# Performance work log

Hardware: AMD Instinct MI355X
Metric: run time of the kernel (lower is better)

Reference implementation:

```python
import jax, jax.numpy as jnp
import numpy as np

N_HEADS = 16
D_MODEL = 1024


def setup_inputs() -> dict:
    key = jax.random.key(0)
    ks = jax.random.split(key, 9)
    B, S, D = 2, 2048, D_MODEL
    scale = 1.0 / np.sqrt(D)
    inp = {
        "x": jax.random.normal(ks[0], (B, S, D), dtype=jnp.float32),
        "wq": jax.random.normal(ks[1], (D, D), dtype=jnp.float32) * scale,
        "bq": jax.random.normal(ks[2], (D,), dtype=jnp.float32) * 0.01,
        "wk": jax.random.normal(ks[3], (D, D), dtype=jnp.float32) * scale,
        "bk": jax.random.normal(ks[4], (D,), dtype=jnp.float32) * 0.01,
        "wv": jax.random.normal(ks[5], (D, D), dtype=jnp.float32) * scale,
        "bv": jax.random.normal(ks[6], (D,), dtype=jnp.float32) * 0.01,
        "wo": jax.random.normal(ks[7], (D, D), dtype=jnp.float32) * scale,
        "bo": jax.random.normal(ks[8], (D,), dtype=jnp.float32) * 0.01,
    }
    return inp


def reference(x, wq, bq, wk, bk, wv, bv, wo, bo):
    B, S, D = x.shape
    H = N_HEADS
    hd = D // H
    # projections -> [B, H, S, hd]
    def proj(w, b):
        return (x @ w + b).reshape(B, S, H, hd).transpose(0, 2, 1, 3)
    q = proj(wq, bq)
    k = proj(wk, bk)
    v = proj(wv, bv)
    scores = jnp.einsum("bhqd,bhkd->bhqk", q, k) * (1.0 / np.sqrt(hd))
    # causal mask: future tokens (col > row) -> -inf
    causal = jnp.tril(jnp.ones((S, S), dtype=bool))  # True = allowed
    scores = jnp.where(causal[None, None, :, :], scores, -jnp.inf)
    att = jax.nn.softmax(scores, axis=-1)
    y = jnp.einsum("bhqk,bhkd->bhqd", att, v)  # [B,H,S,hd]
    y = y.transpose(0, 2, 1, 3).reshape(B, S, D)
    return y @ wo + bo
```

## Files before the change

kernel.cpp:

```cpp
#include <hip/hip_runtime.h>
#include <hip/hip_bf16.h>
#include <math.h>

typedef unsigned short u16;
typedef __bf16 bf16x8 __attribute__((ext_vector_type(8)));
typedef short s16x4 __attribute__((ext_vector_type(4)));
typedef float f32x4 __attribute__((ext_vector_type(4)));
typedef u16 u16x8 __attribute__((ext_vector_type(8)));
typedef u16 u16x4 __attribute__((ext_vector_type(4)));

#define DM 1024
#define NH 16
#define SL 2048
#define BB 2
#define TOK (BB * SL)

__device__ __forceinline__ u16 f2bf(float f) {
  union { float f; unsigned u; } v; v.f = f;
  unsigned r = v.u + 0x7FFFu + ((v.u >> 16) & 1u);
  return (u16)(r >> 16);
}

__device__ __forceinline__ float fexp2(float x) {
  float r; asm("v_exp_f32 %0, %1" : "=v"(r) : "v"(x)); return r;
}

__device__ __forceinline__ unsigned cvtpk(float lo, float hi) {
  unsigned r;
  asm("v_cvt_pk_bf16_f32 %0, %1, %2" : "=v"(r) : "v"(lo), "v"(hi));
  return r;
}

__device__ __forceinline__ float max3f(float a, float b, float c) {
  return fmaxf(fmaxf(a, b), c);
}

__device__ __forceinline__ f32x4 pv_mfma(s16x4 a, s16x4 b, f32x4 c) {
#if __has_builtin(__builtin_amdgcn_mfma_f32_16x16x16bf16_1k)
  return __builtin_amdgcn_mfma_f32_16x16x16bf16_1k(a, b, c, 0, 0, 0);
#else
  asm("v_mfma_f32_16x16x16_bf16 %0, %1, %2, %0" : "+v"(c) : "v"(a), "v"(b));
  return c;
#endif
}

typedef __attribute__((address_space(1))) const unsigned GU;
typedef __attribute__((address_space(3))) unsigned LU;
#define GLOAD16(g, l) __builtin_amdgcn_global_load_lds((GU*)(g), (LU*)(l), 16, 0, 0)

__global__ __launch_bounds__(256) void prep(
    const float* __restrict__ x,
    const float* __restrict__ w0, const float* __restrict__ w1,
    const float* __restrict__ w2, const float* __restrict__ w3,
    u16* __restrict__ Xb, u16* __restrict__ Wall) {
  __shared__ u16 T[64][72];
  int bid = blockIdx.x;
  int tid = threadIdx.x;
  if (bid < 1024) {
    int mat = bid >> 8;
    const float* in = (mat == 0) ? w0 : (mat == 1) ? w1 : (mat == 2) ? w2 : w3;
    u16* o = Wall + ((size_t)mat << 20);
    int t2 = bid & 255;
    int k0 = (t2 & 15) * 64, n0 = (t2 >> 4) * 64;
    int r = tid >> 2;
    int c0 = (tid & 3) * 16;
#pragma unroll
    for (int j = 0; j < 16; j += 4) {
      float4 f = *(const float4*)(in + (size_t)(k0 + r) * 1024 + n0 + c0 + j);
      T[c0 + j + 0][r] = f2bf(f.x);
      T[c0 + j + 1][r] = f2bf(f.y);
      T[c0 + j + 2][r] = f2bf(f.z);
      T[c0 + j + 3][r] = f2bf(f.w);
    }
    __syncthreads();
    int n = tid >> 2, k1 = (tid & 3) * 16;
#pragma unroll
    for (int j = 0; j < 16; j += 8)
      *(u16x8*)(o + (size_t)(n0 + n) * 1024 + k0 + k1 + j) = *(const u16x8*)&T[n][k1 + j];
  } else {
    int i = ((bid - 1024) * 256 + tid) * 8;
    float4 a = *(const float4*)(x + i);
    float4 b = *(const float4*)(x + i + 4);
    u16x8 o;
    o[0]=f2bf(a.x); o[1]=f2bf(a.y); o[2]=f2bf(a.z); o[3]=f2bf(a.w);
    o[4]=f2bf(b.x); o[5]=f2bf(b.y); o[6]=f2bf(b.z); o[7]=f2bf(b.w);
    *(u16x8*)(Xb + i) = o;
  }
}

template<int MODE, int BM>
__global__ __launch_bounds__(256) void gemm_qkv(
    const u16* __restrict__ A, const u16* __restrict__ Bt,
    const float* __restrict__ b0, const float* __restrict__ b1,
    const float* __restrict__ b2,
    u16* __restrict__ Qo, u16* __restrict__ Ko, u16* __restrict__ Vto,
    float* __restrict__ Fo)
{
  constexpr int MREP = BM / 32;
  __shared__ u16 As[3][BM * 32];
  __shared__ u16 Bs[3][128 * 32];
  const int tid = threadIdx.x, lane = tid & 63, w = tid >> 6;
  const int fr = lane & 15, fq = lane >> 4;
  const int wr = w >> 1, wc = w & 1;
  const int m0 = blockIdx.x * BM;
  const int n0 = blockIdx.y * 128;
  f32x4 acc[MREP][4] = {};

  auto stage = [&](int buf, int k0) {
#pragma unroll
    for (int i = 0; i < BM / 64; ++i) {
      int b16 = i * 256 + tid;
      int row = b16 >> 2, ch = b16 & 3;
      GLOAD16(A + (size_t)(m0 + row) * DM + k0 + ((ch ^ (row & 3)) * 8), &As[buf][b16 * 8]);
    }
#pragma unroll
    for (int i = 0; i < 2; ++i) {
      int b16 = i * 256 + tid;
      int row = b16 >> 2, ch = b16 & 3;
      GLOAD16(Bt + (size_t)(n0 + row) * DM + k0 + ((ch ^ (row & 3)) * 8), &Bs[buf][b16 * 8]);
    }
  };

  const int NK = DM / 32;
  stage(0, 0);
  stage(1, 32);
  for (int j = 0; j < NK; ++j) {
    if (j + 1 < NK) {
      if constexpr (BM == 128) asm volatile("s_waitcnt vmcnt(4)" ::: "memory");
      else                     asm volatile("s_waitcnt vmcnt(3)" ::: "memory");
    } else {
      asm volatile("s_waitcnt vmcnt(0)" ::: "memory");
    }
    __builtin_amdgcn_s_barrier();
    __builtin_amdgcn_sched_barrier(0);

    const u16* Al = As[j % 3];
    const u16* Bl = Bs[j % 3];
    bf16x8 av[MREP], bv[4];
#pragma unroll
    for (int m = 0; m < MREP; ++m) {
      int row = wr * (BM / 2) + m * 16 + fr;
      av[m] = *(const bf16x8*)&Al[row * 32 + ((fq ^ (row & 3)) * 8)];
    }
#pragma unroll
    for (int n = 0; n < 4; ++n) {
      int row = wc * 64 + n * 16 + fr;
      bv[n] = *(const bf16x8*)&Bl[row * 32 + ((fq ^ (row & 3)) * 8)];
    }
    __builtin_amdgcn_s_setprio(1);
#pragma unroll
    for (int m = 0; m < MREP; ++m)
#pragma unroll
      for (int n = 0; n < 4; ++n)
        acc[m][n] = __builtin_amdgcn_mfma_f32_16x16x32_bf16(av[m], bv[n], acc[m][n], 0, 0, 0);
    __builtin_amdgcn_s_setprio(0);

    if (j + 2 < NK) stage((j + 2) % 3, (j + 2) * 32);
  }

  if (MODE == 0) {
    int nloc = n0 & 1023;
    int mat = n0 >> 10;
    const float* bias = (mat == 0) ? b0 : ((mat == 1) ? b1 : b2);
    const float scl = (mat == 0) ? 0.18033688f : 1.0f;
#pragma unroll
    for (int m = 0; m < MREP; ++m) {
      int row = m0 + wr * (BM / 2) + m * 16 + fq * 4;
#pragma unroll
      for (int n = 0; n < 4; ++n) {
        int col = nloc + wc * 64 + n * 16 + fr;
        float bc = bias[col];
        if (mat == 2) {
          u16x4 v4;
#pragma unroll
          for (int r = 0; r < 4; ++r) v4[r] = f2bf(acc[m][n][r] + bc);
          *(u16x4*)(Vto + (size_t)col * TOK + row) = v4;
        } else {
          u16* dst = (mat == 0) ? Qo : Ko;
#pragma unroll
          for (int r = 0; r < 4; ++r)
            dst[(size_t)(row + r) * DM + col] = f2bf((acc[m][n][r] + bc) * scl);
        }
      }
    }
  } else {
#pragma unroll
    for (int m = 0; m < MREP; ++m) {
      int row = m0 + wr * (BM / 2) + m * 16 + fq * 4;
#pragma unroll
      for (int n = 0; n < 4; ++n) {
        int col = n0 + wc * 64 + n * 16 + fr;
        float bc = b0[col];
#pragma unroll
        for (int r = 0; r < 4; ++r)
          Fo[(size_t)(row + r) * DM + col] = acc[m][n][r] + bc;
      }
    }
  }
}

__global__ __launch_bounds__(256, 4) void attn_kernel(
    const u16* __restrict__ Qg, const u16* __restrict__ Kg,
    const u16* __restrict__ Vt, u16* __restrict__ Og)
{
  __shared__ u16 SM[16384];
  const int tid = threadIdx.x, lane = tid & 63, w = tid >> 6;
  const int fr = lane & 15, fq = lane >> 4;
  const int bid = blockIdx.x;
  const int bh = bid & 31;
  const int g = (bid >> 5) & 7;
  const int kq = bid >> 8;
  const int qt = (kq == 0) ? (31 - g) : (kq == 1) ? (16 + g)
               : (kq == 2) ? (15 - g) : g;
  const int b = bh >> 4, h = bh & 15;
  const size_t rowbase = (size_t)b * SL;
  const int nt = qt + 1;

  const int qrow = qt * 64 + w * 16 + fr;
  bf16x8 qa[2];
#pragma unroll
  for (int c = 0; c < 2; ++c)
    qa[c] = *(const bf16x8*)(Qg + (rowbase + qrow) * DM + h * 64 + c * 32 + fq * 8);

  s16x4 ones1;
  { union { u16 u[4]; s16x4 s; } t1;
    t1.u[0] = 0x3F80; t1.u[1] = 0x3F80; t1.u[2] = 0x3F80; t1.u[3] = 0x3F80;
    ones1 = t1.s; }

  float mrow = -INFINITY;
  f32x4 osum = {};
  f32x4 o[4] = {};

  auto stage = [&](int buf, int t) {
#pragma unroll
    for (int i = 0; i < 2; ++i) {
      int b16 = i * 256 + tid;
      int row = b16 >> 3, ch = b16 & 7;
      GLOAD16(Kg + (rowbase + t * 64 + row) * DM + h * 64 + ((ch ^ (row & 7)) * 8),
              &SM[buf * 4096 + b16 * 8]);
    }
#pragma unroll
    for (int i = 0; i < 2; ++i) {
      int b16 = i * 256 + tid;
      int row = b16 >> 3, ch = b16 & 7;
      GLOAD16(Vt + (size_t)(h * 64 + row) * TOK + b * SL + t * 64 + ((ch ^ (row & 7)) * 8),
              &SM[8192 + buf * 4096 + b16 * 8]);
    }
  };

  stage(0, 0);
  __syncthreads();
  int buf = 0;

  for (int t = 0; t < nt; ++t) {
    if (t + 1 < nt) stage(buf ^ 1, t + 1);
    const u16* Kl = &SM[buf * 4096];
    const u16* Vl = &SM[8192 + buf * 4096];

    f32x4 st[4];
    __builtin_amdgcn_s_setprio(1);
#pragma unroll
    for (int kb = 0; kb < 4; ++kb) {
      int row = kb * 16 + fr;
      bf16x8 kf0 = *(const bf16x8*)&Kl[row * 64 + ((fq ^ (row & 7)) * 8)];
      bf16x8 kf1 = *(const bf16x8*)&Kl[row * 64 + (((4 + fq) ^ (row & 7)) * 8)];
      f32x4 s0 = {};
      s0 = __builtin_amdgcn_mfma_f32_16x16x32_bf16(kf0, qa[0], s0, 0, 0, 0);
      st[kb] = __builtin_amdgcn_mfma_f32_16x16x32_bf16(kf1, qa[1], s0, 0, 0, 0);
    }
    __builtin_amdgcn_s_setprio(0);

    if (t == qt) {
      const int kvb = t * 64 + fq * 4;
#pragma unroll
      for (int kb = 0; kb < 4; ++kb)
#pragma unroll
        for (int r = 0; r < 4; ++r)
          if (kvb + kb * 16 + r > qrow) st[kb][r] = -INFINITY;
    }

    float pa = max3f(st[0][0], st[0][1], st[0][2]);
    float pb = max3f(st[0][3], st[1][0], st[1][1]);
    float pc = max3f(st[1][2], st[1][3], st[2][0]);
    float pd = max3f(st[2][1], st[2][2], st[2][3]);
    float pe = max3f(st[3][0], st[3][1], st[3][2]);
    float pm = max3f(max3f(pa, pb, pc), max3f(pd, pe, st[3][3]), -INFINITY);
    pm = fmaxf(pm, __shfl_xor(pm, 16, 64));
    pm = fmaxf(pm, __shfl_xor(pm, 32, 64));

    if (__any(pm > mrow + 8.f)) {
      float nm = fmaxf(mrow, pm);
      float alpha = fexp2(mrow - nm);
      mrow = nm;
#pragma unroll
      for (int r = 0; r < 4; ++r) osum[r] *= alpha;
#pragma unroll
      for (int db = 0; db < 4; ++db)
#pragma unroll
        for (int r = 0; r < 4; ++r) o[db][r] *= alpha;
    }

    unsigned pk2[4][2];
#pragma unroll
    for (int kb = 0; kb < 4; ++kb) {
      float p0 = fexp2(st[kb][0] - mrow);
      float p1 = fexp2(st[kb][1] - mrow);
      float p2 = fexp2(st[kb][2] - mrow);
      float p3 = fexp2(st[kb][3] - mrow);
      pk2[kb][0] = cvtpk(p0, p1);
      pk2[kb][1] = cvtpk(p2, p3);
    }

    __builtin_amdgcn_s_setprio(1);
#pragma unroll
    for (int kb = 0; kb < 4; ++kb) {
      union { unsigned u[2]; s16x4 s; } bb;
      bb.u[0] = pk2[kb][0]; bb.u[1] = pk2[kb][1];
      osum = pv_mfma(ones1, bb.s, osum);
#pragma unroll
      for (int db = 0; db < 4; ++db) {
        int row = db * 16 + fr;
        s16x4 vfr = *(const s16x4*)&Vl[row * 64 + (((kb * 2 + (fq >> 1)) ^ (row & 7)) * 8) + ((fq & 1) * 4)];
        o[db] = pv_mfma(vfr, bb.s, o[db]);
      }
    }
    __builtin_amdgcn_s_setprio(0);

    __syncthreads();
    buf ^= 1;
  }

  float inv = 1.0f / osum[0];

  u16* Tb = &SM[w * 1152];
#pragma unroll
  for (int db = 0; db < 4; ++db)
#pragma unroll
    for (int w2 = 0; w2 < 2; ++w2) {
      unsigned pk = cvtpk(o[db][2 * w2] * inv, o[db][2 * w2 + 1] * inv);
      *(unsigned*)&Tb[fr * 72 + db * 16 + fq * 4 + 2 * w2] = pk;
    }
  int rr = lane >> 2, cc = (lane & 3) * 16;
  size_t gbase = (rowbase + qt * 64 + w * 16 + rr) * DM + h * 64 + cc;
#pragma unroll
  for (int j2 = 0; j2 < 2; ++j2)
    *(u16x8*)(Og + gbase + j2 * 8) = *(const u16x8*)&Tb[rr * 72 + cc + j2 * 8];
}

extern "C" void kernel_launch(void* const* d_in, const int* in_sizes, int n_in,
                              void* d_out, int out_size, void* d_ws, size_t ws_size,
                              hipStream_t stream) {
  const float* x  = (const float*)d_in[0];
  const float* wq = (const float*)d_in[1];
  const float* bq = (const float*)d_in[2];
  const float* wk = (const float*)d_in[3];
  const float* bk = (const float*)d_in[4];
  const float* wv = (const float*)d_in[5];
  const float* bv = (const float*)d_in[6];
  const float* wo = (const float*)d_in[7];
  const float* bo = (const float*)d_in[8];

  char* ws = (char*)d_ws;
  u16* Xb   = (u16*)ws;
  u16* Wall = (u16*)(ws + 8u  * 1024 * 1024);
  u16* Qb   = (u16*)(ws + 16u * 1024 * 1024);
  u16* Kb   = (u16*)(ws + 24u * 1024 * 1024);
  u16* VtG  = (u16*)(ws + 32u * 1024 * 1024);

  hipLaunchKernelGGL(prep, dim3(1024 + 2048), dim3(256), 0, stream,
                     x, wq, wk, wv, wo, Xb, Wall);

  hipLaunchKernelGGL((gemm_qkv<0, 128>), dim3(TOK / 128, 3072 / 128), dim3(256), 0, stream,
                     Xb, Wall, bq, bk, bv, Qb, Kb, VtG, (float*)nullptr);

  hipLaunchKernelGGL(attn_kernel, dim3(32 * BB * NH), dim3(256), 0, stream,
                     Qb, Kb, VtG, Xb);

  hipLaunchKernelGGL((gemm_qkv<1, 64>), dim3(TOK / 64, DM / 128), dim3(256), 0, stream,
                     Xb, Wall + 3u * (1u << 20), bo, (const float*)nullptr, (const float*)nullptr,
                     (u16*)nullptr, (u16*)nullptr, (u16*)nullptr, (float*)d_out);
}
```

Baseline: 101.0 us.

## Use 128x64 tiles with K=16 MFMA for the QKV projection GEMM

The QKV projection GEMM moves from a 128x128 tile with K-step 32 (16x16x32 bf16 MFMA) to a 128x64 tile with K-step 16, using the smaller pv_mfma (16x16x16 style) and a new 1-bit XOR swizzle. This doubles the number of blocks (32x48 grid) so more CUs stay busy, at the cost of lower data reuse per tile, twice as many K iterations with barriers, and a less efficient MFMA shape. The output GEMM is split into its own non-templated kernel with the same behaviour as before.

```diff
diff --git a/kernel.cpp b/kernel.cpp
--- a/kernel.cpp
+++ b/kernel.cpp
@@ -88,15 +88,98 @@
   }
 }
 
-template<int MODE, int BM>
-__global__ __launch_bounds__(256) void gemm_qkv(
+__global__ __launch_bounds__(256) void gemm_qkv16(
     const u16* __restrict__ A, const u16* __restrict__ Bt,
     const float* __restrict__ b0, const float* __restrict__ b1,
     const float* __restrict__ b2,
-    u16* __restrict__ Qo, u16* __restrict__ Ko, u16* __restrict__ Vto,
-    float* __restrict__ Fo)
+    u16* __restrict__ Qo, u16* __restrict__ Ko, u16* __restrict__ Vto)
 {
-  constexpr int MREP = BM / 32;
+  __shared__ u16 As[3][128 * 16];
+  __shared__ u16 Bs[3][64 * 16];
+  const int tid = threadIdx.x, lane = tid & 63, w = tid >> 6;
+  const int fr = lane & 15, fq = lane >> 4;
+  const int wr = w >> 1, wc = w & 1;
+  const int m0 = blockIdx.x * 128;
+  const int n0 = blockIdx.y * 64;
+  f32x4 acc[4][2] = {};
+
+  auto stage = [&](int buf, int k0) {
+    {
+      int row = tid >> 1, ch = tid & 1;
+      GLOAD16(A + (size_t)(m0 + row) * DM + k0 + ((ch ^ (row & 1)) * 8), &As[buf][tid * 8]);
+    }
+    if (tid < 128) {
+      int row = tid >> 1, ch = tid & 1;
+      GLOAD16(Bt + (size_t)(n0 + row) * DM + k0 + ((ch ^ (row & 1)) * 8), &Bs[buf][tid * 8]);
+    }
+  };
+
+  const int NK = DM / 16;
+  stage(0, 0);
+  stage(1, 16);
+  for (int j = 0; j < NK; ++j) {
+    if (j + 1 < NK) asm volatile("s_waitcnt vmcnt(1)" ::: "memory");
+    else            asm volatile("s_waitcnt vmcnt(0)" ::: "memory");
+    __builtin_amdgcn_s_barrier();
+    __builtin_amdgcn_sched_barrier(0);
+
+    const u16* Al = As[j % 3];
+    const u16* Bl = Bs[j % 3];
+    s16x4 av[4], bv[2];
+#pragma unroll
+    for (int m = 0; m < 4; ++m) {
+      int row = wr * 64 + m * 16 + fr;
+      av[m] = *(const s16x4*)&Al[row * 16 + (((fq >> 1) ^ (row & 1)) * 8) + (fq & 1) * 4];
+    }
+#pragma unroll
+    for (int n = 0; n < 2; ++n) {
+      int row = wc * 32 + n * 16 + fr;
+      bv[n] = *(const s16x4*)&Bl[row * 16 + (((fq >> 1) ^ (row & 1)) * 8) + (fq & 1) * 4];
+    }
+    __builtin_amdgcn_s_setprio(1);
+#pragma unroll
+    for (int m = 0; m < 4; ++m)
+#pragma unroll
+      for (int n = 0; n < 2; ++n)
+        acc[m][n] = pv_mfma(av[m], bv[n], acc[m][n]);
+    __builtin_amdgcn_s_setprio(0);
+
+    if (j + 2 < NK) stage((j + 2) % 3, (j + 2) * 16);
+  }
+
+  {
+    int nloc = n0 & 1023;
+    int mat = n0 >> 10;
+    const float* bias = (mat == 0) ? b0 : ((mat == 1) ? b1 : b2);
+    const float scl = (mat == 0) ? 0.18033688f : 1.0f;
+#pragma unroll
+    for (int m = 0; m < 4; ++m) {
+      int row = m0 + wr * 64 + m * 16 + fq * 4;
+#pragma unroll
+      for (int n = 0; n < 2; ++n) {
+        int col = nloc + wc * 32 + n * 16 + fr;
+        float bc = bias[col];
+        if (mat == 2) {
+          u16x4 v4;
+#pragma unroll
+          for (int r = 0; r < 4; ++r) v4[r] = f2bf(acc[m][n][r] + bc);
+          *(u16x4*)(Vto + (size_t)col * TOK + row) = v4;
+        } else {
+          u16* dst = (mat == 0) ? Qo : Ko;
+#pragma unroll
+          for (int r = 0; r < 4; ++r)
+            dst[(size_t)(row + r) * DM + col] = f2bf((acc[m][n][r] + bc) * scl);
+        }
+      }
+    }
+  }
+}
+
+__global__ __launch_bounds__(256) void gemm_out(
+    const u16* __restrict__ A, const u16* __restrict__ Bt,
+    const float* __restrict__ b0, float* __restrict__ Fo)
+{
+  constexpr int BM = 64, MREP = 2;
   __shared__ u16 As[3][BM * 32];
   __shared__ u16 Bs[3][128 * 32];
   const int tid = threadIdx.x, lane = tid & 63, w = tid >> 6;
@@ -107,9 +190,8 @@
   f32x4 acc[MREP][4] = {};
 
   auto stage = [&](int buf, int k0) {
-#pragma unroll
-    for (int i = 0; i < BM / 64; ++i) {
-      int b16 = i * 256 + tid;
+    {
+      int b16 = tid;
       int row = b16 >> 2, ch = b16 & 3;
       GLOAD16(A + (size_t)(m0 + row) * DM + k0 + ((ch ^ (row & 3)) * 8), &As[buf][b16 * 8]);
     }
@@ -125,12 +207,8 @@
   stage(0, 0);
   stage(1, 32);
   for (int j = 0; j < NK; ++j) {
-    if (j + 1 < NK) {
-      if constexpr (BM == 128) asm volatile("s_waitcnt vmcnt(4)" ::: "memory");
-      else                     asm volatile("s_waitcnt vmcnt(3)" ::: "memory");
-    } else {
-      asm volatile("s_waitcnt vmcnt(0)" ::: "memory");
-    }
+    if (j + 1 < NK) asm volatile("s_waitcnt vmcnt(3)" ::: "memory");
+    else            asm volatile("s_waitcnt vmcnt(0)" ::: "memory");
     __builtin_amdgcn_s_barrier();
     __builtin_amdgcn_sched_barrier(0);
 
@@ -158,43 +236,16 @@
     if (j + 2 < NK) stage((j + 2) % 3, (j + 2) * 32);
   }
 
-  if (MODE == 0) {
-    int nloc = n0 & 1023;
-    int mat = n0 >> 10;
-    const float* bias = (mat == 0) ? b0 : ((mat == 1) ? b1 : b2);
-    const float scl = (mat == 0) ? 0.18033688f : 1.0f;
-#pragma unroll
-    for (int m = 0; m < MREP; ++m) {
-      int row = m0 + wr * (BM / 2) + m * 16 + fq * 4;
-#pragma unroll
-      for (int n = 0; n < 4; ++n) {
-        int col = nloc + wc * 64 + n * 16 + fr;
-        float bc = bias[col];
-        if (mat == 2) {
-          u16x4 v4;
-#pragma unroll
-          for (int r = 0; r < 4; ++r) v4[r] = f2bf(acc[m][n][r] + bc);
-          *(u16x4*)(Vto + (size_t)col * TOK + row) = v4;
-        } else {
-          u16* dst = (mat == 0) ? Qo : Ko;
-#pragma unroll
-          for (int r = 0; r < 4; ++r)
-            dst[(size_t)(row + r) * DM + col] = f2bf((acc[m][n][r] + bc) * scl);
-        }
-      }
-    }
-  } else {
-#pragma unroll
-    for (int m = 0; m < MREP; ++m) {
-      int row = m0 + wr * (BM / 2) + m * 16 + fq * 4;
-#pragma unroll
-      for (int n = 0; n < 4; ++n) {
-        int col = n0 + wc * 64 + n * 16 + fr;
-        float bc = b0[col];
-#pragma unroll
-        for (int r = 0; r < 4; ++r)
-          Fo[(size_t)(row + r) * DM + col] = acc[m][n][r] + bc;
-      }
+#pragma unroll
+  for (int m = 0; m < MREP; ++m) {
+    int row = m0 + wr * (BM / 2) + m * 16 + fq * 4;
+#pragma unroll
+    for (int n = 0; n < 4; ++n) {
+      int col = n0 + wc * 64 + n * 16 + fr;
+      float bc = b0[col];
+#pragma unroll
+      for (int r = 0; r < 4; ++r)
+        Fo[(size_t)(row + r) * DM + col] = acc[m][n][r] + bc;
     }
   }
 }
@@ -370,13 +421,12 @@
   hipLaunchKernelGGL(prep, dim3(1024 + 2048), dim3(256), 0, stream,
                      x, wq, wk, wv, wo, Xb, Wall);
 
-  hipLaunchKernelGGL((gemm_qkv<0, 128>), dim3(TOK / 128, 3072 / 128), dim3(256), 0, stream,
-                     Xb, Wall, bq, bk, bv, Qb, Kb, VtG, (float*)nullptr);
+  hipLaunchKernelGGL(gemm_qkv16, dim3(TOK / 128, 3072 / 64), dim3(256), 0, stream,
+                     Xb, Wall, bq, bk, bv, Qb, Kb, VtG);
 
   hipLaunchKernelGGL(attn_kernel, dim3(32 * BB * NH), dim3(256), 0, stream,
                      Qb, Kb, VtG, Xb);
 
-  hipLaunchKernelGGL((gemm_qkv<1, 64>), dim3(TOK / 64, DM / 128), dim3(256), 0, stream,
-                     Xb, Wall + 3u * (1u << 20), bo, (const float*)nullptr, (const float*)nullptr,
-                     (u16*)nullptr, (u16*)nullptr, (u16*)nullptr, (float*)d_out);
-}
+  hipLaunchKernelGGL(gemm_out, dim3(TOK / 64, DM / 128), dim3(256), 0, stream,
+                     Xb, Wall + 3u * (1u << 20), bo, (float*)d_out);
+}
```

Result: slower. 142.1 us (+40.7%).

## Pre-tile V into MFMA fragment order for contiguous loads

Applied to the files above, without the earlier changes.

The QKV projection epilogue now writes V into per-(batch, head, kv-tile) 4096-element blocks, arranged so that each lane's PV MFMA operands for two kb steps sit in one contiguous 16-byte chunk. The attention kernel then stages V tiles with fully linear global loads and reads them from LDS with one 128-bit load per two MFMAs, replacing swizzled 64-bit reads. This is meant to cut LDS read instructions and address arithmetic in the inner loop. In exchange, the projection's V stores become more scattered 8-byte writes.

```diff
diff --git a/kernel.cpp b/kernel.cpp
--- a/kernel.cpp
+++ b/kernel.cpp
@@ -174,7 +174,15 @@
           u16x4 v4;
 #pragma unroll
           for (int r = 0; r < 4; ++r) v4[r] = f2bf(acc[m][n][r] + bc);
-          *(u16x4*)(Vto + (size_t)col * TOK + row) = v4;
+          int bp   = row >> 11;
+          int tkv  = (row & 2047) >> 6;
+          int kvin = row & 63;
+          int kb   = kvin >> 4, fqv = (kvin >> 2) & 3;
+          int hh   = col >> 6, dh = col & 63;
+          int db2  = dh >> 4;
+          size_t base = (((size_t)bp * NH + hh) * 32 + tkv) * 4096;
+          int off = (db2 * 2 + (kb >> 1)) * 512 + (fqv * 16 + (dh & 15)) * 8 + (kb & 1) * 4;
+          *(u16x4*)(Vto + base + off) = v4;
         } else {
           u16* dst = (mat == 0) ? Qo : Ko;
 #pragma unroll
@@ -227,6 +235,8 @@
     t1.u[0] = 0x3F80; t1.u[1] = 0x3F80; t1.u[2] = 0x3F80; t1.u[3] = 0x3F80;
     ones1 = t1.s; }
 
+  const size_t vtile0 = (((size_t)b * NH + h) * 32) * 4096;
+
   float mrow = -INFINITY;
   f32x4 osum = {};
   f32x4 o[4] = {};
@@ -241,10 +251,9 @@
     }
 #pragma unroll
     for (int i = 0; i < 2; ++i) {
-      int b16 = i * 256 + tid;
-      int row = b16 >> 3, ch = b16 & 7;
-      GLOAD16(Vt + (size_t)(h * 64 + row) * TOK + b * SL + t * 64 + ((ch ^ (row & 7)) * 8),
-              &SM[8192 + buf * 4096 + b16 * 8]);
+      int c16 = i * 256 + tid;
+      GLOAD16(Vt + vtile0 + (size_t)t * 4096 + c16 * 8,
+              &SM[8192 + buf * 4096 + c16 * 8]);
     }
   };
 
@@ -313,15 +322,18 @@
 
     __builtin_amdgcn_s_setprio(1);
 #pragma unroll
-    for (int kb = 0; kb < 4; ++kb) {
-      union { unsigned u[2]; s16x4 s; } bb;
-      bb.u[0] = pk2[kb][0]; bb.u[1] = pk2[kb][1];
-      osum = pv_mfma(ones1, bb.s, osum);
+    for (int j = 0; j < 2; ++j) {
+      union { unsigned u[2]; s16x4 s; } bb0, bb1;
+      bb0.u[0] = pk2[2 * j][0];     bb0.u[1] = pk2[2 * j][1];
+      bb1.u[0] = pk2[2 * j + 1][0]; bb1.u[1] = pk2[2 * j + 1][1];
+      osum = pv_mfma(ones1, bb0.s, osum);
+      osum = pv_mfma(ones1, bb1.s, osum);
 #pragma unroll
       for (int db = 0; db < 4; ++db) {
-        int row = db * 16 + fr;
-        s16x4 vfr = *(const s16x4*)&Vl[row * 64 + (((kb * 2 + (fq >> 1)) ^ (row & 7)) * 8) + ((fq & 1) * 4)];
-        o[db] = pv_mfma(vfr, bb.s, o[db]);
+        union { bf16x8 v; s16x4 s2[2]; } vv;
+        vv.v = *(const bf16x8*)&Vl[(db * 2 + j) * 512 + lane * 8];
+        o[db] = pv_mfma(vv.s2[0], bb0.s, o[db]);
+        o[db] = pv_mfma(vv.s2[1], bb1.s, o[db]);
       }
     }
     __builtin_amdgcn_s_setprio(0);
```

Result: faster. 95.06 us (median of 2 runs) (-5.9%).
